# Kernel optimization log

Hardware: AMD Instinct MI355X
Metric: run time of the kernel (lower is better)

The kernel has to match this reference:

```python
import jax, jax.numpy as jnp
import numpy as np

HEAD_DIM = 64
HIDDEN_SIZE = 3072
NUM_HEADS = 48
B, TXT, VID = 1, 256, 1792
N = TXT + VID


def _layernorm(x, g, b, eps=1e-5):
    mu = jnp.mean(x, axis=-1, keepdims=True)
    xc = x - mu
    var = jnp.mean(xc * xc, axis=-1, keepdims=True)
    return xc * jax.lax.rsqrt(var + eps) * g + b


def _apply_rope1(x, freqs):
    # x: [B, L, H, D]; freqs: [1, 1, Lf, D//2, 2, 2]
    Bx, L, H, D = x.shape
    x_ = x.reshape(Bx, L, H, D // 2, 1, 2)
    # faithful to torch: if dim-2 sizes mismatch (H vs Lf), slice freqs to H
    if x_.shape[2] != 1 and freqs.shape[2] != 1 and x_.shape[2] != freqs.shape[2]:
        freqs = freqs[:, :, : x_.shape[2]]
    out = freqs[..., 0] * x_[..., 0] + freqs[..., 1] * x_[..., 1]
    return out.reshape(Bx, L, H, D).astype(x.dtype)


def setup_inputs() -> dict:
    key = jax.random.key(0)
    ks = jax.random.split(key, 16)
    s = 1.0 / np.sqrt(HIDDEN_SIZE)
    d = dict(
        combined=jax.random.normal(ks[0], (B, N, HIDDEN_SIZE), jnp.float32),
        freqs=jax.random.normal(ks[1], (1, 1, VID, HEAD_DIM // 2, 2, 2), jnp.float32),
        Wq=jax.random.normal(ks[2], (HIDDEN_SIZE, HIDDEN_SIZE), jnp.float32) * s,
        bq=jnp.zeros((HIDDEN_SIZE,), jnp.float32),
        Wk=jax.random.normal(ks[3], (HIDDEN_SIZE, HIDDEN_SIZE), jnp.float32) * s,
        bk=jnp.zeros((HIDDEN_SIZE,), jnp.float32),
        Wv=jax.random.normal(ks[4], (HIDDEN_SIZE, HIDDEN_SIZE), jnp.float32) * s,
        bv=jnp.zeros((HIDDEN_SIZE,), jnp.float32),
        Wo=jax.random.normal(ks[5], (HIDDEN_SIZE, HIDDEN_SIZE), jnp.float32) * s,
        bo=jnp.zeros((HIDDEN_SIZE,), jnp.float32),
        gq=jnp.ones((HEAD_DIM,), jnp.float32),
        bgq=jnp.zeros((HEAD_DIM,), jnp.float32),
        gk=jnp.ones((HEAD_DIM,), jnp.float32),
        bgk=jnp.zeros((HEAD_DIM,), jnp.float32),
        txt_len=TXT,
    )
    return d


def reference(combined, freqs, Wq, bq, Wk, bk, Wv, bv, Wo, bo, gq, bgq, gk, bgk, txt_len):
    Bx, Nx, _ = combined.shape
    Q = (combined @ Wq.T + bq).reshape(Bx, Nx, NUM_HEADS, HEAD_DIM)
    K = (combined @ Wk.T + bk).reshape(Bx, Nx, NUM_HEADS, HEAD_DIM)
    V = (combined @ Wv.T + bv).reshape(Bx, Nx, NUM_HEADS, HEAD_DIM)
    Q = _layernorm(Q, gq, bgq)
    K = _layernorm(K, gk, bgk)
    if freqs is not None and Nx - txt_len > 0:
        Q_vid = _apply_rope1(Q[:, txt_len:], freqs)
        K_vid = _apply_rope1(K[:, txt_len:], freqs)
        Q = jnp.concatenate([Q[:, :txt_len], Q_vid], axis=1)
        K = jnp.concatenate([K[:, :txt_len], K_vid], axis=1)
    # SDPA in fp32: [B, H, N, D]
    q = Q.transpose(0, 2, 1, 3).astype(jnp.float32)
    k = K.transpose(0, 2, 1, 3).astype(jnp.float32)
    v = V.transpose(0, 2, 1, 3).astype(jnp.float32)
    scale = 1.0 / np.sqrt(HEAD_DIM)
    scores = jnp.einsum('bhqd,bhkd->bhqk', q, k) * scale
    probs = jax.nn.softmax(scores, axis=-1)
    attn = jnp.einsum('bhqk,bhkd->bhqd', probs, v).astype(combined.dtype)
    attn = attn.transpose(0, 2, 1, 3).reshape(Bx, Nx, HIDDEN_SIZE)
    out = attn @ Wo.T + bo
    return out[:, txt_len:], out[:, :txt_len]
```

## Files before the change

### kernel.cpp

```cpp
#include <hip/hip_runtime.h>
#include <hip/hip_bf16.h>

typedef __attribute__((ext_vector_type(8))) short bf16x8;
typedef __attribute__((ext_vector_type(4))) float f32x4;
typedef unsigned int __attribute__((address_space(1))) as1_uint;
typedef unsigned int __attribute__((address_space(3))) as3_uint;

#define TXT 256
#define VIDN 1792
#define SEQ 2048
#define HID 3072
#define NH 48
#define HD 64
#define QSCALE 0.18033688011112042f

__device__ __forceinline__ unsigned short f2bf(float f) {
  union { float f; unsigned int u; } x; x.f = f;
  unsigned int r = x.u + 0x7fffu + ((x.u >> 16) & 1u);
  return (unsigned short)(r >> 16);
}

__device__ __forceinline__ void gload16(const void* g, void* l) {
  __builtin_amdgcn_global_load_lds((const as1_uint*)g, (as3_uint*)l, 16, 0, 0);
}

__device__ __forceinline__ void fbar() {
  asm volatile("" ::: "memory");
  __builtin_amdgcn_s_barrier();
  asm volatile("" ::: "memory");
}

__global__ __launch_bounds__(256) void cvt_kernel(const float* __restrict__ s,
                                                  unsigned short* __restrict__ d, int n) {
  int i = (blockIdx.x * 256 + threadIdx.x) * 4;
  if (i >= n) return;
  float4 v = *(const float4*)(s + i);
  ushort4 o;
  o.x = f2bf(v.x); o.y = f2bf(v.y); o.z = f2bf(v.z); o.w = f2bf(v.w);
  *(ushort4*)(d + i) = o;
}

__global__ __launch_bounds__(256) void cvt4_kernel(
    const float* __restrict__ comb, const float* __restrict__ wq,
    const float* __restrict__ wk, const float* __restrict__ wv,
    unsigned short* __restrict__ abf, unsigned short* __restrict__ wqkv) {
  const int CB = (SEQ * HID) / 1024;
  const int WB = (HID * HID) / 1024;
  int bid = blockIdx.x;
  const float* s; unsigned short* d; int r;
  if (bid < CB) { s = comb; d = abf; r = bid; }
  else {
    int q = bid - CB; int m = q / WB; r = q - m * WB;
    s = (m == 0) ? wq : (m == 1) ? wk : wv;
    d = wqkv + (size_t)m * HID * HID;
  }
  int i = (r * 256 + threadIdx.x) * 4;
  float4 v = *(const float4*)(s + i);
  ushort4 o;
  o.x = f2bf(v.x); o.y = f2bf(v.y); o.z = f2bf(v.z); o.w = f2bf(v.w);
  *(ushort4*)(d + i) = o;
}

template<int MODE>
__global__ __launch_bounds__(512) void gemm8p(
    const unsigned short* __restrict__ A,
    const unsigned short* __restrict__ Bt,
    int K, int ntn,
    float* __restrict__ Cq, unsigned short* __restrict__ Vt, const float* __restrict__ bv,
    float* __restrict__ Cout, const float* __restrict__ bo)
{
  __shared__ unsigned short lds[3 * 24576];
  const int tid = threadIdx.x;
  const int mt = blockIdx.x / ntn, nt = blockIdx.x % ntn;
  const int m0 = mt * 128, n0 = nt * 256;
  const int w = tid >> 6, lane = tid & 63, lr = lane & 15, lg = lane >> 4;
  const int wr = w >> 2, wc = w & 3;
  f32x4 acc[4][4] = {};
  const int NT = K >> 6;

  const unsigned short *As0, *As1, *Bs0, *Bs1, *Bs2, *Bs3;
  int ao0, ao1, bb0, bb1, bb2, bb3;
  {
    int so, ss;
    so = tid * 16;          ss = so ^ (((so >> 7) & 7) << 4);
    ao0 = so; As0 = A + (size_t)(m0 + (ss >> 7)) * K + ((ss & 127) >> 1);
    so = (512 + tid) * 16;  ss = so ^ (((so >> 7) & 7) << 4);
    ao1 = so; As1 = A + (size_t)(m0 + (ss >> 7)) * K + ((ss & 127) >> 1);
    so = tid * 16;          ss = so ^ (((so >> 7) & 7) << 4);
    bb0 = so; Bs0 = Bt + (size_t)(n0 + (ss >> 7)) * K + ((ss & 127) >> 1);
    so = (512 + tid) * 16;  ss = so ^ (((so >> 7) & 7) << 4);
    bb1 = so; Bs1 = Bt + (size_t)(n0 + (ss >> 7)) * K + ((ss & 127) >> 1);
    so = (1024 + tid) * 16; ss = so ^ (((so >> 7) & 7) << 4);
    bb2 = so; Bs2 = Bt + (size_t)(n0 + (ss >> 7)) * K + ((ss & 127) >> 1);
    so = (1536 + tid) * 16; ss = so ^ (((so >> 7) & 7) << 4);
    bb3 = so; Bs3 = Bt + (size_t)(n0 + (ss >> 7)) * K + ((ss & 127) >> 1);
  }

  int ra[2][4], rb[2][4];
#pragma unroll
  for (int h = 0; h < 2; ++h) {
#pragma unroll
    for (int f = 0; f < 4; ++f) {
      int r1 = wr * 64 + f * 16 + lr;
      ra[h][f] = (r1 * 64 + h * 32 + lg * 8) ^ ((r1 & 7) << 3);
      int r2 = wc * 64 + f * 16 + lr;
      rb[h][f] = (r2 * 64 + h * 32 + lg * 8) ^ ((r2 & 7) << 3);
    }
  }

#define STAGE_ALL(t)                                                           \
  {                                                                            \
    char* sb_ = (char*)lds + ((t) % 3) * 49152;                                \
    const int kk_ = (t) << 6;                                                  \
    gload16(As0 + kk_, sb_ + ao0);                                             \
    gload16(As1 + kk_, sb_ + ao1);                                             \
    gload16(Bs0 + kk_, sb_ + 16384 + bb0);                                     \
    gload16(Bs1 + kk_, sb_ + 16384 + bb1);                                     \
    gload16(Bs2 + kk_, sb_ + 16384 + bb2);                                     \
    gload16(Bs3 + kk_, sb_ + 16384 + bb3);                                     \
  }

#define MM8(N0, N1)                                                            \
  __builtin_amdgcn_s_setprio(1);                                               \
  acc[0][N0] = __builtin_amdgcn_mfma_f32_16x16x32_bf16(af0, bq0, acc[0][N0], 0, 0, 0); \
  acc[1][N0] = __builtin_amdgcn_mfma_f32_16x16x32_bf16(af1, bq0, acc[1][N0], 0, 0, 0); \
  acc[2][N0] = __builtin_amdgcn_mfma_f32_16x16x32_bf16(af2, bq0, acc[2][N0], 0, 0, 0); \
  acc[3][N0] = __builtin_amdgcn_mfma_f32_16x16x32_bf16(af3, bq0, acc[3][N0], 0, 0, 0); \
  acc[0][N1] = __builtin_amdgcn_mfma_f32_16x16x32_bf16(af0, bq1, acc[0][N1], 0, 0, 0); \
  acc[1][N1] = __builtin_amdgcn_mfma_f32_16x16x32_bf16(af1, bq1, acc[1][N1], 0, 0, 0); \
  acc[2][N1] = __builtin_amdgcn_mfma_f32_16x16x32_bf16(af2, bq1, acc[2][N1], 0, 0, 0); \
  acc[3][N1] = __builtin_amdgcn_mfma_f32_16x16x32_bf16(af3, bq1, acc[3][N1], 0, 0, 0); \
  __builtin_amdgcn_s_setprio(0);

#define ITER(t, SG, VMC)                                                       \
  {                                                                            \
    const unsigned short* lA = lds + ((t) % 3) * 24576;                        \
    const unsigned short* lB = lA + 8192;                                      \
    char* sb = (char*)lds + (((t) + 2) % 3) * 49152;                           \
    const int kk = ((t) + 2) << 6;                                             \
    bf16x8 af0, af1, af2, af3, bq0, bq1;                                       \
                                                \
    af0 = *(const bf16x8*)&lA[ra[0][0]];                                       \
    af1 = *(const bf16x8*)&lA[ra[0][1]];                                       \
    af2 = *(const bf16x8*)&lA[ra[0][2]];                                       \
    af3 = *(const bf16x8*)&lA[ra[0][3]];                                       \
    bq0 = *(const bf16x8*)&lB[rb[0][0]];                                       \
    bq1 = *(const bf16x8*)&lB[rb[0][1]];                                       \
    if (SG) { gload16(As0 + kk, sb + ao0); gload16(As1 + kk, sb + ao1); }      \
    fbar();                                                                    \
    MM8(0, 1)                                                                  \
    fbar();                                                                    \
                                                \
    bq0 = *(const bf16x8*)&lB[rb[0][2]];                                       \
    bq1 = *(const bf16x8*)&lB[rb[0][3]];                                       \
    if (SG) { gload16(Bs0 + kk, sb + 16384 + bb0);                             \
              gload16(Bs1 + kk, sb + 16384 + bb1); }                           \
    fbar();                                                                    \
    MM8(2, 3)                                                                  \
    fbar();                                                                    \
                                                \
    af0 = *(const bf16x8*)&lA[ra[1][0]];                                       \
    af1 = *(const bf16x8*)&lA[ra[1][1]];                                       \
    af2 = *(const bf16x8*)&lA[ra[1][2]];                                       \
    af3 = *(const bf16x8*)&lA[ra[1][3]];                                       \
    bq0 = *(const bf16x8*)&lB[rb[1][0]];                                       \
    bq1 = *(const bf16x8*)&lB[rb[1][1]];                                       \
    if (SG) { gload16(Bs2 + kk, sb + 16384 + bb2);                             \
              gload16(Bs3 + kk, sb + 16384 + bb3); }                           \
    fbar();                                                                    \
    MM8(0, 1)                                                                  \
    fbar();                                                                    \
                      \
    bq0 = *(const bf16x8*)&lB[rb[1][2]];                                       \
    bq1 = *(const bf16x8*)&lB[rb[1][3]];                                       \
    VMC;                                                                       \
    fbar();                                                                    \
    MM8(2, 3)                                                                  \
    fbar();                                                                    \
  }

  STAGE_ALL(0);
  STAGE_ALL(1);
  asm volatile("s_waitcnt vmcnt(6)" ::: "memory");
  fbar();
  int t = 0;
  for (; t < NT - 2; ++t)
    ITER(t, 1, asm volatile("s_waitcnt vmcnt(6)" ::: "memory"));
  ITER(t, 0, asm volatile("s_waitcnt vmcnt(0)" ::: "memory"));
  ++t;
  ITER(t, 0, ((void)0));
#undef STAGE_ALL
#undef MM8
#undef ITER

  if (MODE == 0) {
    if (n0 < 6144) {
#pragma unroll
      for (int mf = 0; mf < 4; ++mf) {
        int row = m0 + wr * 64 + mf * 16 + lg * 4;
#pragma unroll
        for (int nf = 0; nf < 4; ++nf) {
          int col = n0 + wc * 64 + nf * 16 + lr;
#pragma unroll
          for (int j = 0; j < 4; ++j)
            Cq[(size_t)(row + j) * 6144 + col] = acc[mf][nf][j];
        }
      }
    } else {
#pragma unroll
      for (int mf = 0; mf < 4; ++mf) {
        int srow2 = m0 + wr * 64 + mf * 16 + lg * 4;
#pragma unroll
        for (int nf = 0; nf < 4; ++nf) {
          int n2 = n0 - 6144 + wc * 64 + nf * 16 + lr;
          float b = bv[n2];
          ushort4 pk;
          pk.x = f2bf(acc[mf][nf][0] + b);
          pk.y = f2bf(acc[mf][nf][1] + b);
          pk.z = f2bf(acc[mf][nf][2] + b);
          pk.w = f2bf(acc[mf][nf][3] + b);
          *(ushort4*)(Vt + (size_t)n2 * SEQ + srow2) = pk;
        }
      }
    }
  } else {
#pragma unroll
    for (int mf = 0; mf < 4; ++mf) {
      int row = m0 + wr * 64 + mf * 16 + lg * 4;
#pragma unroll
      for (int nf = 0; nf < 4; ++nf) {
        int col = n0 + wc * 64 + nf * 16 + lr;
        float b = bo[col];
#pragma unroll
        for (int j = 0; j < 4; ++j) {
          int s = row + j;
          int orow = (s >= TXT) ? (s - TXT) : (VIDN + s);
          Cout[(size_t)orow * HID + col] = acc[mf][nf][j] + b;
        }
      }
    }
  }
}

__global__ __launch_bounds__(256) void ln_rope_kernel(
    const float* __restrict__ QK,
    const float* __restrict__ bq, const float* __restrict__ bk,
    const float* __restrict__ gq, const float* __restrict__ bgq,
    const float* __restrict__ gk, const float* __restrict__ bgk,
    const float* __restrict__ freqs,
    unsigned short* __restrict__ Qh, unsigned short* __restrict__ Kh)
{
  int wid = blockIdx.x * 4 + (threadIdx.x >> 6);
  int lane = threadIdx.x & 63;
  int s = wid / 96;
  int rem = wid - s * 96;
  int h = rem >> 1, qk = rem & 1;
  int col = h * 64 + lane;
  float x = QK[(size_t)s * 6144 + qk * 3072 + col] + (qk ? bk[col] : bq[col]);
  float m = x;
#pragma unroll
  for (int msk = 1; msk < 64; msk <<= 1) m += __shfl_xor(m, msk);
  float mu = m * (1.0f / 64.0f);
  float xc = x - mu;
  float v = xc * xc;
#pragma unroll
  for (int msk = 1; msk < 64; msk <<= 1) v += __shfl_xor(v, msk);
  float rstd = rsqrtf(v * (1.0f / 64.0f) + 1e-5f);
  float y = xc * rstd * (qk ? gk[lane] : gq[lane]) + (qk ? bgk[lane] : bgq[lane]);
  if (s >= TXT) {
    float p = __shfl_xor(y, 1);
    float xe = (lane & 1) ? p : y;
    float xo = (lane & 1) ? y : p;
    int base = h * 128 + (lane >> 1) * 4 + (lane & 1) * 2;
    y = freqs[base] * xe + freqs[base + 1] * xo;
  }
  if (!qk) y *= QSCALE;
  (qk ? Kh : Qh)[((size_t)h * SEQ + s) * 64 + lane] = f2bf(y);
}

__global__ __launch_bounds__(512) void fattn_kernel(
    const unsigned short* __restrict__ Qh, const unsigned short* __restrict__ Kh,
    const unsigned short* __restrict__ Vt, unsigned short* __restrict__ ctx)
{
  __shared__ unsigned short kt[2][2][64][32];
  __shared__ unsigned short vt[2][2][64][32];
  __shared__ unsigned short pl[8][16][72];
  const int h = blockIdx.x >> 4;
  const int q0 = (blockIdx.x & 15) * 128;
  const int tid = threadIdx.x, w = tid >> 6, lane = tid & 63, lr = lane & 15, lg = lane >> 4;

  bf16x8 qf0, qf1;
  {
    const unsigned short* qp = Qh + ((size_t)h * SEQ + q0 + w * 16 + lr) * 64 + lg * 8;
    qf0 = *(const bf16x8*)qp;
    qf1 = *(const bf16x8*)(qp + 32);
  }
  f32x4 oacc[4] = {};
  float mrun = -1e30f, lrun = 0.f;

  const int soff = tid * 16;
  const int shalf = soff >> 12;
  const int srem = soff & 4095;
  const int srow = srem >> 6, scb = srem & 63;
  const unsigned short* Ksrc = Kh + ((size_t)h * SEQ + srow) * 64 + shalf * 32 + (scb >> 1);
  const unsigned short* Vsrc = Vt + ((size_t)(h * 64 + srow)) * SEQ + shalf * 32 + (scb >> 1);

#define FSTAGE(t)                                                              \
  {                                                                            \
    const int sl_ = (t) & 1;                                                   \
    const int kv0_ = (t) << 6;                                                 \
    gload16(Ksrc + (size_t)kv0_ * 64, (char*)kt + sl_ * 8192 + soff);          \
    gload16(Vsrc + kv0_, (char*)vt + sl_ * 8192 + soff);                       \
  }

  FSTAGE(0);
  for (int t = 0; t < 32; ++t) {
    const int sl = t & 1;
    if (t < 31) {
      FSTAGE(t + 1);
      asm volatile("s_waitcnt vmcnt(2)" ::: "memory");
    } else {
      asm volatile("s_waitcnt vmcnt(0)" ::: "memory");
    }
    fbar();

    f32x4 sacc[4] = {};
    __builtin_amdgcn_s_setprio(1);
#pragma unroll
    for (int nf = 0; nf < 4; ++nf) {
      bf16x8 a0 = *(const bf16x8*)&kt[sl][0][nf * 16 + lr][lg * 8];
      bf16x8 a1 = *(const bf16x8*)&kt[sl][1][nf * 16 + lr][lg * 8];
      sacc[nf] = __builtin_amdgcn_mfma_f32_16x16x32_bf16(a0, qf0, sacc[nf], 0, 0, 0);
      sacc[nf] = __builtin_amdgcn_mfma_f32_16x16x32_bf16(a1, qf1, sacc[nf], 0, 0, 0);
    }
    __builtin_amdgcn_s_setprio(0);

    float mx;
    {
      float t0 = fmaxf(fmaxf(sacc[0][0], sacc[0][1]), fmaxf(sacc[0][2], sacc[0][3]));
      float t1 = fmaxf(fmaxf(sacc[1][0], sacc[1][1]), fmaxf(sacc[1][2], sacc[1][3]));
      float t2 = fmaxf(fmaxf(sacc[2][0], sacc[2][1]), fmaxf(sacc[2][2], sacc[2][3]));
      float t3 = fmaxf(fmaxf(sacc[3][0], sacc[3][1]), fmaxf(sacc[3][2], sacc[3][3]));
      mx = fmaxf(fmaxf(t0, t1), fmaxf(t2, t3));
    }
    mx = fmaxf(mx, __shfl_xor(mx, 16));
    mx = fmaxf(mx, __shfl_xor(mx, 32));

    if (!__all(mx <= mrun + 8.0f)) {
      float mn = fmaxf(mrun, mx);
      float corr = exp2f(mrun - mn);
      lrun *= corr;
      mrun = mn;
      float c0 = __shfl(corr, lg * 4 + 0);
      float c1 = __shfl(corr, lg * 4 + 1);
      float c2 = __shfl(corr, lg * 4 + 2);
      float c3 = __shfl(corr, lg * 4 + 3);
#pragma unroll
      for (int df = 0; df < 4; ++df) {
        oacc[df][0] *= c0; oacc[df][1] *= c1;
        oacc[df][2] *= c2; oacc[df][3] *= c3;
      }
    }

    float pr[4][4];
#pragma unroll
    for (int nf = 0; nf < 4; ++nf)
#pragma unroll
      for (int r = 0; r < 4; ++r)
        pr[nf][r] = exp2f(sacc[nf][r] - mrun);
    float rs;
    {
      float s0 = (pr[0][0] + pr[0][1]) + (pr[0][2] + pr[0][3]);
      float s1 = (pr[1][0] + pr[1][1]) + (pr[1][2] + pr[1][3]);
      float s2 = (pr[2][0] + pr[2][1]) + (pr[2][2] + pr[2][3]);
      float s3 = (pr[3][0] + pr[3][1]) + (pr[3][2] + pr[3][3]);
      rs = (s0 + s1) + (s2 + s3);
    }
    rs += __shfl_xor(rs, 16);
    rs += __shfl_xor(rs, 32);
    lrun += rs;

#pragma unroll
    for (int nf = 0; nf < 4; ++nf) {
      union { __hip_bfloat162 h; unsigned int u; } c0, c1;
      c0.h = __float22bfloat162_rn(make_float2(pr[nf][0], pr[nf][1]));
      c1.h = __float22bfloat162_rn(make_float2(pr[nf][2], pr[nf][3]));
      uint2 pw; pw.x = c0.u; pw.y = c1.u;
      *(uint2*)&pl[w][lr][nf * 16 + lg * 4] = pw;
    }

    bf16x8 pa0 = *(const bf16x8*)&pl[w][lr][lg * 8];
    bf16x8 pa1 = *(const bf16x8*)&pl[w][lr][32 + lg * 8];
    __builtin_amdgcn_s_setprio(1);
#pragma unroll
    for (int df = 0; df < 4; ++df) {
      bf16x8 v0 = *(const bf16x8*)&vt[sl][0][df * 16 + lr][lg * 8];
      bf16x8 v1 = *(const bf16x8*)&vt[sl][1][df * 16 + lr][lg * 8];
      oacc[df] = __builtin_amdgcn_mfma_f32_16x16x32_bf16(pa0, v0, oacc[df], 0, 0, 0);
      oacc[df] = __builtin_amdgcn_mfma_f32_16x16x32_bf16(pa1, v1, oacc[df], 0, 0, 0);
    }
    __builtin_amdgcn_s_setprio(0);

    fbar();
  }
#undef FSTAGE

  float linv = 1.0f / lrun;
  float i0 = __shfl(linv, lg * 4 + 0);
  float i1 = __shfl(linv, lg * 4 + 1);
  float i2 = __shfl(linv, lg * 4 + 2);
  float i3 = __shfl(linv, lg * 4 + 3);
#pragma unroll
  for (int df = 0; df < 4; ++df) {
    int s = q0 + w * 16 + lg * 4;
    int dcol = h * 64 + df * 16 + lr;
    ctx[(size_t)(s + 0) * HID + dcol] = f2bf(oacc[df][0] * i0);
    ctx[(size_t)(s + 1) * HID + dcol] = f2bf(oacc[df][1] * i1);
    ctx[(size_t)(s + 2) * HID + dcol] = f2bf(oacc[df][2] * i2);
    ctx[(size_t)(s + 3) * HID + dcol] = f2bf(oacc[df][3] * i3);
  }
}

extern "C" void kernel_launch(void* const* d_in, const int* in_sizes, int n_in,
                              void* d_out, int out_size, void* d_ws, size_t ws_size,
                              hipStream_t stream) {
  const float* combined = (const float*)d_in[0];
  const float* freqs    = (const float*)d_in[1];
  const float* Wq  = (const float*)d_in[2];
  const float* bq  = (const float*)d_in[3];
  const float* Wk  = (const float*)d_in[4];
  const float* bk  = (const float*)d_in[5];
  const float* Wv  = (const float*)d_in[6];
  const float* bv  = (const float*)d_in[7];
  const float* Wo  = (const float*)d_in[8];
  const float* bo  = (const float*)d_in[9];
  const float* gq  = (const float*)d_in[10];
  const float* bgq = (const float*)d_in[11];
  const float* gk  = (const float*)d_in[12];
  const float* bgk = (const float*)d_in[13];
  float* out = (float*)d_out;

  char* ws = (char*)d_ws;
  unsigned short* Abf  = (unsigned short*)ws; ws += (size_t)SEQ * HID * 2;
  unsigned short* Wqkv = (unsigned short*)ws; ws += (size_t)3 * HID * HID * 2;
  float*          QK   = (float*)ws;          ws += (size_t)SEQ * 6144 * 4;
  unsigned short* Qh   = (unsigned short*)ws; ws += (size_t)NH * SEQ * HD * 2;
  unsigned short* Kh   = (unsigned short*)ws; ws += (size_t)NH * SEQ * HD * 2;
  unsigned short* Vt   = (unsigned short*)ws; ws += (size_t)NH * HD * SEQ * 2;
  unsigned short* Wob  = (unsigned short*)QK;
  unsigned short* ctx  = Abf;

  cvt4_kernel<<<(SEQ * HID) / 1024 + 3 * (HID * HID) / 1024, 256, 0, stream>>>(
      combined, Wq, Wk, Wv, Abf, Wqkv);

  gemm8p<0><<<16 * 36, 512, 0, stream>>>(Abf, Wqkv, HID, 36, QK, Vt, bv, nullptr, nullptr);

  ln_rope_kernel<<<(SEQ * NH * 2) / 4, 256, 0, stream>>>(QK, bq, bk, gq, bgq, gk, bgk, freqs, Qh, Kh);

  cvt_kernel<<<(HID * HID) / 1024, 256, 0, stream>>>(Wo, Wob, HID * HID);

  fattn_kernel<<<NH * 16, 512, 0, stream>>>(Qh, Kh, Vt, ctx);

  gemm8p<1><<<16 * 12, 512, 0, stream>>>(ctx, Wob, HID, 12, nullptr, nullptr, nullptr, out, bo);
}
```

Before: 403.2 us.

## Process two query tiles per flash-attention block to reuse K/V tiles

Each attention block now handles 256 queries (two 128-query groups per wave set) instead of 128, halving the grid to NH*8 blocks. Every K/V tile loaded into LDS is consumed by two independent softmax/MFMA groups, which halves global K/V traffic and barrier count per query. The cost is higher register pressure from doubled accumulators and Q fragments, and fewer blocks (384) for the 256 CUs, which may hurt occupancy and load balance.

```diff
diff --git a/kernel.cpp b/kernel.cpp
--- a/kernel.cpp
+++ b/kernel.cpp
@@ -285,18 +285,21 @@
   __shared__ unsigned short kt[2][2][64][32];
   __shared__ unsigned short vt[2][2][64][32];
   __shared__ unsigned short pl[8][16][72];
-  const int h = blockIdx.x >> 4;
-  const int q0 = (blockIdx.x & 15) * 128;
+  const int h = blockIdx.x >> 3;
+  const int q0 = (blockIdx.x & 7) * 256;
   const int tid = threadIdx.x, w = tid >> 6, lane = tid & 63, lr = lane & 15, lg = lane >> 4;
 
-  bf16x8 qf0, qf1;
+  bf16x8 qfA0, qfA1, qfB0, qfB1;
   {
     const unsigned short* qp = Qh + ((size_t)h * SEQ + q0 + w * 16 + lr) * 64 + lg * 8;
-    qf0 = *(const bf16x8*)qp;
-    qf1 = *(const bf16x8*)(qp + 32);
-  }
-  f32x4 oacc[4] = {};
-  float mrun = -1e30f, lrun = 0.f;
+    qfA0 = *(const bf16x8*)qp;
+    qfA1 = *(const bf16x8*)(qp + 32);
+    qp += (size_t)128 * 64;
+    qfB0 = *(const bf16x8*)qp;
+    qfB1 = *(const bf16x8*)(qp + 32);
+  }
+  f32x4 oaccA[4] = {}, oaccB[4] = {};
+  float mrunA = -1e30f, lrunA = 0.f, mrunB = -1e30f, lrunB = 0.f;
 
   const int soff = tid * 16;
   const int shalf = soff >> 12;
@@ -311,6 +314,81 @@
     const int kv0_ = (t) << 6;                                                 \
     gload16(Ksrc + (size_t)kv0_ * 64, (char*)kt + sl_ * 8192 + soff);          \
     gload16(Vsrc + kv0_, (char*)vt + sl_ * 8192 + soff);                       \
+  }
+
+#define GROUP(QF0, QF1, OACC, MRUN, LRUN)                                      \
+  {                                                                            \
+    f32x4 sacc[4] = {};                                                        \
+    __builtin_amdgcn_s_setprio(1);                                             \
+    _Pragma("unroll")                                                          \
+    for (int nf = 0; nf < 4; ++nf) {                                           \
+      bf16x8 a0 = *(const bf16x8*)&kt[sl][0][nf * 16 + lr][lg * 8];            \
+      bf16x8 a1 = *(const bf16x8*)&kt[sl][1][nf * 16 + lr][lg * 8];            \
+      sacc[nf] = __builtin_amdgcn_mfma_f32_16x16x32_bf16(a0, QF0, sacc[nf], 0, 0, 0); \
+      sacc[nf] = __builtin_amdgcn_mfma_f32_16x16x32_bf16(a1, QF1, sacc[nf], 0, 0, 0); \
+    }                                                                          \
+    __builtin_amdgcn_s_setprio(0);                                             \
+    float mx;                                                                  \
+    {                                                                          \
+      float t0 = fmaxf(fmaxf(sacc[0][0], sacc[0][1]), fmaxf(sacc[0][2], sacc[0][3])); \
+      float t1 = fmaxf(fmaxf(sacc[1][0], sacc[1][1]), fmaxf(sacc[1][2], sacc[1][3])); \
+      float t2 = fmaxf(fmaxf(sacc[2][0], sacc[2][1]), fmaxf(sacc[2][2], sacc[2][3])); \
+      float t3 = fmaxf(fmaxf(sacc[3][0], sacc[3][1]), fmaxf(sacc[3][2], sacc[3][3])); \
+      mx = fmaxf(fmaxf(t0, t1), fmaxf(t2, t3));                                \
+    }                                                                          \
+    mx = fmaxf(mx, __shfl_xor(mx, 16));                                        \
+    mx = fmaxf(mx, __shfl_xor(mx, 32));                                        \
+    if (!__all(mx <= MRUN + 8.0f)) {                                           \
+      float mn = fmaxf(MRUN, mx);                                              \
+      float corr = exp2f(MRUN - mn);                                           \
+      LRUN *= corr;                                                            \
+      MRUN = mn;                                                               \
+      float c0 = __shfl(corr, lg * 4 + 0);                                     \
+      float c1 = __shfl(corr, lg * 4 + 1);                                     \
+      float c2 = __shfl(corr, lg * 4 + 2);                                     \
+      float c3 = __shfl(corr, lg * 4 + 3);                                     \
+      _Pragma("unroll")                                                        \
+      for (int df = 0; df < 4; ++df) {                                         \
+        OACC[df][0] *= c0; OACC[df][1] *= c1;                                  \
+        OACC[df][2] *= c2; OACC[df][3] *= c3;                                  \
+      }                                                                        \
+    }                                                                          \
+    float pr[4][4];                                                            \
+    _Pragma("unroll")                                                          \
+    for (int nf = 0; nf < 4; ++nf)                                             \
+      _Pragma("unroll")                                                        \
+      for (int r = 0; r < 4; ++r)                                              \
+        pr[nf][r] = exp2f(sacc[nf][r] - MRUN);                                 \
+    float rs;                                                                  \
+    {                                                                          \
+      float s0 = (pr[0][0] + pr[0][1]) + (pr[0][2] + pr[0][3]);                \
+      float s1 = (pr[1][0] + pr[1][1]) + (pr[1][2] + pr[1][3]);                \
+      float s2 = (pr[2][0] + pr[2][1]) + (pr[2][2] + pr[2][3]);                \
+      float s3 = (pr[3][0] + pr[3][1]) + (pr[3][2] + pr[3][3]);                \
+      rs = (s0 + s1) + (s2 + s3);                                              \
+    }                                                                          \
+    rs += __shfl_xor(rs, 16);                                                  \
+    rs += __shfl_xor(rs, 32);                                                  \
+    LRUN += rs;                                                                \
+    _Pragma("unroll")                                                          \
+    for (int nf = 0; nf < 4; ++nf) {                                           \
+      union { __hip_bfloat162 h; unsigned int u; } c0, c1;                     \
+      c0.h = __float22bfloat162_rn(make_float2(pr[nf][0], pr[nf][1]));         \
+      c1.h = __float22bfloat162_rn(make_float2(pr[nf][2], pr[nf][3]));         \
+      uint2 pw; pw.x = c0.u; pw.y = c1.u;                                      \
+      *(uint2*)&pl[w][lr][nf * 16 + lg * 4] = pw;                              \
+    }                                                                          \
+    bf16x8 pa0 = *(const bf16x8*)&pl[w][lr][lg * 8];                           \
+    bf16x8 pa1 = *(const bf16x8*)&pl[w][lr][32 + lg * 8];                      \
+    __builtin_amdgcn_s_setprio(1);                                             \
+    _Pragma("unroll")                                                          \
+    for (int df = 0; df < 4; ++df) {                                           \
+      bf16x8 v0 = *(const bf16x8*)&vt[sl][0][df * 16 + lr][lg * 8];            \
+      bf16x8 v1 = *(const bf16x8*)&vt[sl][1][df * 16 + lr][lg * 8];            \
+      OACC[df] = __builtin_amdgcn_mfma_f32_16x16x32_bf16(pa0, v0, OACC[df], 0, 0, 0); \
+      OACC[df] = __builtin_amdgcn_mfma_f32_16x16x32_bf16(pa1, v1, OACC[df], 0, 0, 0); \
+    }                                                                          \
+    __builtin_amdgcn_s_setprio(0);                                             \
   }
 
   FSTAGE(0);
@@ -323,101 +401,44 @@
       asm volatile("s_waitcnt vmcnt(0)" ::: "memory");
     }
     fbar();
-
-    f32x4 sacc[4] = {};
-    __builtin_amdgcn_s_setprio(1);
-#pragma unroll
-    for (int nf = 0; nf < 4; ++nf) {
-      bf16x8 a0 = *(const bf16x8*)&kt[sl][0][nf * 16 + lr][lg * 8];
-      bf16x8 a1 = *(const bf16x8*)&kt[sl][1][nf * 16 + lr][lg * 8];
-      sacc[nf] = __builtin_amdgcn_mfma_f32_16x16x32_bf16(a0, qf0, sacc[nf], 0, 0, 0);
-      sacc[nf] = __builtin_amdgcn_mfma_f32_16x16x32_bf16(a1, qf1, sacc[nf], 0, 0, 0);
-    }
-    __builtin_amdgcn_s_setprio(0);
-
-    float mx;
-    {
-      float t0 = fmaxf(fmaxf(sacc[0][0], sacc[0][1]), fmaxf(sacc[0][2], sacc[0][3]));
-      float t1 = fmaxf(fmaxf(sacc[1][0], sacc[1][1]), fmaxf(sacc[1][2], sacc[1][3]));
-      float t2 = fmaxf(fmaxf(sacc[2][0], sacc[2][1]), fmaxf(sacc[2][2], sacc[2][3]));
-      float t3 = fmaxf(fmaxf(sacc[3][0], sacc[3][1]), fmaxf(sacc[3][2], sacc[3][3]));
-      mx = fmaxf(fmaxf(t0, t1), fmaxf(t2, t3));
-    }
-    mx = fmaxf(mx, __shfl_xor(mx, 16));
-    mx = fmaxf(mx, __shfl_xor(mx, 32));
-
-    if (!__all(mx <= mrun + 8.0f)) {
-      float mn = fmaxf(mrun, mx);
-      float corr = exp2f(mrun - mn);
-      lrun *= corr;
-      mrun = mn;
-      float c0 = __shfl(corr, lg * 4 + 0);
-      float c1 = __shfl(corr, lg * 4 + 1);
-      float c2 = __shfl(corr, lg * 4 + 2);
-      float c3 = __shfl(corr, lg * 4 + 3);
-#pragma unroll
-      for (int df = 0; df < 4; ++df) {
-        oacc[df][0] *= c0; oacc[df][1] *= c1;
-        oacc[df][2] *= c2; oacc[df][3] *= c3;
-      }
-    }
-
-    float pr[4][4];
-#pragma unroll
-    for (int nf = 0; nf < 4; ++nf)
-#pragma unroll
-      for (int r = 0; r < 4; ++r)
-        pr[nf][r] = exp2f(sacc[nf][r] - mrun);
-    float rs;
-    {
-      float s0 = (pr[0][0] + pr[0][1]) + (pr[0][2] + pr[0][3]);
-      float s1 = (pr[1][0] + pr[1][1]) + (pr[1][2] + pr[1][3]);
-      float s2 = (pr[2][0] + pr[2][1]) + (pr[2][2] + pr[2][3]);
-      float s3 = (pr[3][0] + pr[3][1]) + (pr[3][2] + pr[3][3]);
-      rs = (s0 + s1) + (s2 + s3);
-    }
-    rs += __shfl_xor(rs, 16);
-    rs += __shfl_xor(rs, 32);
-    lrun += rs;
-
-#pragma unroll
-    for (int nf = 0; nf < 4; ++nf) {
-      union { __hip_bfloat162 h; unsigned int u; } c0, c1;
-      c0.h = __float22bfloat162_rn(make_float2(pr[nf][0], pr[nf][1]));
-      c1.h = __float22bfloat162_rn(make_float2(pr[nf][2], pr[nf][3]));
-      uint2 pw; pw.x = c0.u; pw.y = c1.u;
-      *(uint2*)&pl[w][lr][nf * 16 + lg * 4] = pw;
-    }
-
-    bf16x8 pa0 = *(const bf16x8*)&pl[w][lr][lg * 8];
-    bf16x8 pa1 = *(const bf16x8*)&pl[w][lr][32 + lg * 8];
-    __builtin_amdgcn_s_setprio(1);
+    GROUP(qfA0, qfA1, oaccA, mrunA, lrunA)
+    GROUP(qfB0, qfB1, oaccB, mrunB, lrunB)
+    fbar();
+  }
+#undef FSTAGE
+#undef GROUP
+
+  {
+    float linv = 1.0f / lrunA;
+    float i0 = __shfl(linv, lg * 4 + 0);
+    float i1 = __shfl(linv, lg * 4 + 1);
+    float i2 = __shfl(linv, lg * 4 + 2);
+    float i3 = __shfl(linv, lg * 4 + 3);
 #pragma unroll
     for (int df = 0; df < 4; ++df) {
-      bf16x8 v0 = *(const bf16x8*)&vt[sl][0][df * 16 + lr][lg * 8];
-      bf16x8 v1 = *(const bf16x8*)&vt[sl][1][df * 16 + lr][lg * 8];
-      oacc[df] = __builtin_amdgcn_mfma_f32_16x16x32_bf16(pa0, v0, oacc[df], 0, 0, 0);
-      oacc[df] = __builtin_amdgcn_mfma_f32_16x16x32_bf16(pa1, v1, oacc[df], 0, 0, 0);
-    }
-    __builtin_amdgcn_s_setprio(0);
-
-    fbar();
-  }
-#undef FSTAGE
-
-  float linv = 1.0f / lrun;
-  float i0 = __shfl(linv, lg * 4 + 0);
-  float i1 = __shfl(linv, lg * 4 + 1);
-  float i2 = __shfl(linv, lg * 4 + 2);
-  float i3 = __shfl(linv, lg * 4 + 3);
-#pragma unroll
-  for (int df = 0; df < 4; ++df) {
-    int s = q0 + w * 16 + lg * 4;
-    int dcol = h * 64 + df * 16 + lr;
-    ctx[(size_t)(s + 0) * HID + dcol] = f2bf(oacc[df][0] * i0);
-    ctx[(size_t)(s + 1) * HID + dcol] = f2bf(oacc[df][1] * i1);
-    ctx[(size_t)(s + 2) * HID + dcol] = f2bf(oacc[df][2] * i2);
-    ctx[(size_t)(s + 3) * HID + dcol] = f2bf(oacc[df][3] * i3);
+      int s = q0 + w * 16 + lg * 4;
+      int dcol = h * 64 + df * 16 + lr;
+      ctx[(size_t)(s + 0) * HID + dcol] = f2bf(oaccA[df][0] * i0);
+      ctx[(size_t)(s + 1) * HID + dcol] = f2bf(oaccA[df][1] * i1);
+      ctx[(size_t)(s + 2) * HID + dcol] = f2bf(oaccA[df][2] * i2);
+      ctx[(size_t)(s + 3) * HID + dcol] = f2bf(oaccA[df][3] * i3);
+    }
+  }
+  {
+    float linv = 1.0f / lrunB;
+    float i0 = __shfl(linv, lg * 4 + 0);
+    float i1 = __shfl(linv, lg * 4 + 1);
+    float i2 = __shfl(linv, lg * 4 + 2);
+    float i3 = __shfl(linv, lg * 4 + 3);
+#pragma unroll
+    for (int df = 0; df < 4; ++df) {
+      int s = q0 + 128 + w * 16 + lg * 4;
+      int dcol = h * 64 + df * 16 + lr;
+      ctx[(size_t)(s + 0) * HID + dcol] = f2bf(oaccB[df][0] * i0);
+      ctx[(size_t)(s + 1) * HID + dcol] = f2bf(oaccB[df][1] * i1);
+      ctx[(size_t)(s + 2) * HID + dcol] = f2bf(oaccB[df][2] * i2);
+      ctx[(size_t)(s + 3) * HID + dcol] = f2bf(oaccB[df][3] * i3);
+    }
   }
 }
 
@@ -459,7 +480,7 @@
 
   cvt_kernel<<<(HID * HID) / 1024, 256, 0, stream>>>(Wo, Wob, HID * HID);
 
-  fattn_kernel<<<NH * 16, 512, 0, stream>>>(Qh, Kh, Vt, ctx);
+  fattn_kernel<<<NH * 8, 512, 0, stream>>>(Qh, Kh, Vt, ctx);
 
   gemm8p<1><<<16 * 12, 512, 0, stream>>>(ctx, Wob, HID, 12, nullptr, nullptr, nullptr, out, bo);
 }
```

Measured after the change: 433.5 us. +7.5%, slower.
